# Kernel tuning notes

Hardware: AMD Instinct MI355X
Metric: run time of the kernel (lower is better)

Reference implementation:

```python
import jax, jax.numpy as jnp
import numpy as np
from jax import lax

VOCAB = 50257
S = 96          # seqlen
E = 768         # embedding_dim
H = 768         # lstm hidden
NL = 2          # lstm layers
L = S - 1       # model2 conv blocks (kernel=2, length 96 -> 1)


def setup_inputs() -> dict:
    key = jax.random.key(0)
    ks = jax.random.split(key, 10)
    he = float(np.sqrt(2.0 / (E * 2)))  # He init for kernel-2 relu convs
    return {
        "x": jax.random.randint(ks[0], (1, S), 0, VOCAB),
        "h_state": jnp.zeros((NL, 1, H), jnp.float32),
        "c_state": jnp.zeros((NL, 1, H), jnp.float32),
        "model2_previousOut": jnp.zeros((1, E, 1), jnp.float32),
        "emb1": jax.random.normal(ks[1], (VOCAB, E), jnp.float32),
        "emb2": jax.random.normal(ks[2], (VOCAB, E), jnp.float32),
        "lstm_w_ih": jax.random.normal(ks[3], (NL, 4 * H, E), jnp.float32) * 0.02,
        "lstm_w_hh": jax.random.normal(ks[4], (NL, 4 * H, H), jnp.float32) * 0.02,
        "lstm_b_ih": jnp.zeros((NL, 4 * H), jnp.float32),
        "lstm_b_hh": jnp.zeros((NL, 4 * H), jnp.float32),
        "pred_w": jax.random.normal(ks[5], (1, H * NL), jnp.float32) * 0.02,
        "pred_b": jnp.zeros((1,), jnp.float32),
        "conv_w": jax.random.normal(ks[6], (L, E, E, 2), jnp.float32) * he,
        "conv_b": jnp.zeros((L, E), jnp.float32),
        "m2pred_w": jax.random.normal(ks[7], (1, E, 2), jnp.float32) * 0.02,
        "m2pred_b": jnp.zeros((1,), jnp.float32),
    }


def _lstm_layer(seq, h0, c0, w_ih, w_hh, b_ih, b_hh):
    # seq: [S, in_dim]; torch gate order i, f, g, o
    def step(carry, xt):
        h, c = carry
        g = w_ih @ xt + w_hh @ h + b_ih + b_hh  # [4H]
        i, f, gg, o = jnp.split(g, 4)
        i = jax.nn.sigmoid(i)
        f = jax.nn.sigmoid(f)
        gg = jnp.tanh(gg)
        o = jax.nn.sigmoid(o)
        c = f * c + i * gg
        h = o * jnp.tanh(c)
        return (h, c), h
    (h, c), ys = lax.scan(step, (h0, c0), seq)
    return ys, h, c


def _forward(x, h_state, c_state, model2_previousOut, emb1, emb2,
             lstm_w_ih, lstm_w_hh, lstm_b_ih, lstm_b_hh,
             pred_w, pred_b, conv_w, conv_b, m2pred_w, m2pred_b):
    xb = x[0]                      # [S] token ids (batch=1)
    # ---- model 1: embedding -> 2-layer LSTM -> linear head on final cell states
    seq = emb1[xb]                 # [S, E]
    hs, cs = [], []
    for l in range(NL):
        seq, h, c = _lstm_layer(seq, h_state[l, 0], c_state[l, 0],
                                lstm_w_ih[l], lstm_w_hh[l], lstm_b_ih[l], lstm_b_hh[l])
        hs.append(h)
        cs.append(c)
    h = jnp.stack(hs)[:, None, :]  # [NL, 1, H]
    c = jnp.stack(cs)[:, None, :]  # [NL, 1, H]
    feat = jnp.transpose(c, (1, 2, 0)).reshape(1, H * NL)  # torch permute(1,2,0)+flatten
    out = feat @ pred_w.T + pred_b                          # [1, 1]
    # ---- model 2: embedding -> chain of 95 distinct Conv1d(E,E,2)+ReLU (length 96 -> 1)
    # Fixed-width buffer trick: each layer's position t uses x[t], x[t+1]; only
    # position 0 of the final layer is valid, and it never touches roll wrap-around.
    e2 = emb2[xb].T                # [E, S]
    def cstep(xbuf, wb):
        w, b = wb                  # w: [E, E, 2], b: [E]
        y = jax.nn.relu(w[:, :, 0] @ xbuf + w[:, :, 1] @ jnp.roll(xbuf, -1, axis=1)
                        + b[:, None])
        return y, None
    xbuf, _ = lax.scan(cstep, e2, (conv_w, conv_b))
    model2out = xbuf[None, :, :1]  # [1, E, 1]
    cat = jnp.concatenate([model2out, model2_previousOut], axis=-1)  # [1, E, 2]
    out2 = (jnp.einsum('oek,bek->bo', m2pred_w, cat) + m2pred_b).reshape(1, 1)
    new_prev = model2out.reshape(1, E, 1)
    return out, h, c, out2, new_prev


def reference(x, h_state, c_state, model2_previousOut, emb1, emb2,
              lstm_w_ih, lstm_w_hh, lstm_b_ih, lstm_b_hh,
              pred_w, pred_b, conv_w, conv_b, m2pred_w, m2pred_b):
    return _forward(x, h_state, c_state, model2_previousOut, emb1, emb2,
                    lstm_w_ih, lstm_w_hh, lstm_b_ih, lstm_b_hh,
                    pred_w, pred_b, conv_w, conv_b, m2pred_w, m2pred_b)
```

## Files before the change

kernel.cpp:

```cpp
#include <hip/hip_runtime.h>
#include <math.h>

#define SEQ 96
#define EMB 768
#define G4  3072
#define NLAYER 95
#define CKP 264
#define CONV_WG 48
#define LSTM_WG 192
#define NREP 32
#define XPITCH 1536
#define WB_BYTES 225345536ull

typedef float  f32x4  __attribute__((ext_vector_type(4)));
typedef short  bf16x8 __attribute__((ext_vector_type(8)));
typedef unsigned long long ull;

union BF8 { unsigned short u[8]; bf16x8 v; };

__device__ __forceinline__ unsigned short f2bf(float f) {
    unsigned u = __float_as_uint(f);
    u += 0x7FFFu + ((u >> 16) & 1u);
    return (unsigned short)(u >> 16);
}
__device__ __forceinline__ float bf2f(unsigned short u) {
    return __uint_as_float(((unsigned)u) << 16);
}

__device__ __forceinline__ ull ld64g(const void* p) {
    return __hip_atomic_load((const ull*)p, __ATOMIC_RELAXED,
                             __HIP_MEMORY_SCOPE_AGENT);
}
__device__ __forceinline__ void st32g(void* p, unsigned v) {
    __hip_atomic_store((unsigned*)p, v, __ATOMIC_RELAXED,
                       __HIP_MEMORY_SCOPE_AGENT);
}
__device__ __forceinline__ void stf32g(float* p, float v) {
    __hip_atomic_store((unsigned*)p, __float_as_uint(v), __ATOMIC_RELAXED,
                       __HIP_MEMORY_SCOPE_AGENT);
}
__device__ __forceinline__ unsigned ldflag(const unsigned* p) {
    return __hip_atomic_load(p, __ATOMIC_RELAXED, __HIP_MEMORY_SCOPE_AGENT);
}
__device__ __forceinline__ unsigned ldflag_acq(const unsigned* p) {
    return __hip_atomic_load(p, __ATOMIC_ACQUIRE, __HIP_MEMORY_SCOPE_AGENT);
}
__device__ __forceinline__ void stflag(unsigned* p, unsigned v) {
    __hip_atomic_store(p, v, __ATOMIC_RELAXED, __HIP_MEMORY_SCOPE_AGENT);
}

__device__ __forceinline__ void relbar(unsigned* flags, unsigned* epoch,
                                       int nwg, int wg, unsigned target) {
    asm volatile("s_waitcnt vmcnt(0)" ::: "memory");
    __syncthreads();
    if (threadIdx.x == 0) stflag(&flags[wg * 16], target);
    if (wg == 0) {
        if ((int)threadIdx.x < nwg)
            while (ldflag(&flags[threadIdx.x * 16]) < target)
                __builtin_amdgcn_s_sleep(2);
        __syncthreads();
        if (threadIdx.x < NREP) stflag(&epoch[threadIdx.x * 16], target);
    }
    if (threadIdx.x == 0) {
        const unsigned* ep = &epoch[(wg & (NREP - 1)) * 16];
        while (ldflag(ep) < target)
            __builtin_amdgcn_s_sleep(8);
    }
    asm volatile("" ::: "memory");
    __syncthreads();
}

__device__ __forceinline__ float red16(float a) {
    a += __shfl_xor(a, 8, 16);
    a += __shfl_xor(a, 4, 16);
    a += __shfl_xor(a, 2, 16);
    a += __shfl_xor(a, 1, 16);
    return a;
}

__device__ __forceinline__ float sigmoidf_(float x) {
    return 1.0f / (1.0f + __expf(-x));
}

__global__ void k_prep(const float* __restrict__ w,
                       unsigned short* __restrict__ wb0,
                       unsigned short* __restrict__ wb1) {
    const size_t p0 = ((size_t)blockIdx.x * 256 + threadIdx.x) * 4;
    const f32x4* src = (const f32x4*)(w + p0 * 2);
    f32x4 f0 = __builtin_nontemporal_load(src);
    f32x4 f1 = __builtin_nontemporal_load(src + 1);
    ushort4 a, b;
    a.x = f2bf(f0.x); b.x = f2bf(f0.y);
    a.y = f2bf(f0.z); b.y = f2bf(f0.w);
    a.z = f2bf(f1.x); b.z = f2bf(f1.y);
    a.w = f2bf(f1.z); b.w = f2bf(f1.w);
    *(ushort4*)(wb0 + p0) = a;
    *(ushort4*)(wb1 + p0) = b;
}

__global__ void k_embed(const int* __restrict__ xids,
                        const float* __restrict__ emb2,
                        unsigned short* __restrict__ x0) {
    const int col = blockIdx.x;
    const int tok = xids[col];
    const int tid = threadIdx.x;
    if (tid < 192) {
        float4 v = *(const float4*)(emb2 + (size_t)tok * EMB + tid * 4);
        ushort4 hv, lv;
        hv.x = f2bf(v.x); lv.x = f2bf(v.x - bf2f(hv.x));
        hv.y = f2bf(v.y); lv.y = f2bf(v.y - bf2f(hv.y));
        hv.z = f2bf(v.z); lv.z = f2bf(v.z - bf2f(hv.z));
        hv.w = f2bf(v.w); lv.w = f2bf(v.w - bf2f(hv.w));
        unsigned short* base = x0 + col * XPITCH + (tid >> 2) * 32 + (tid & 3) * 4;
        *(ushort4*)base        = hv;
        *(ushort4*)(base + 16) = lv;
    }
}

#define ISSUE_W_B16(LAY, W0R, W1R) do {                                      \
    const unsigned short* w0_ = wb0 + ((size_t)(LAY) * EMB + r0 + lj) * EMB; \
    const unsigned short* w1_ = wb1 + ((size_t)(LAY) * EMB + r0 + lj) * EMB; \
    _Pragma("unroll")                                                        \
    for (int ch_ = 0; ch_ < 3; ++ch_) {                                      \
        const int k_ = ch_ * 256 + wv * 32 + lg * 8;                         \
        W0R[ch_] = *(const bf16x8*)(w0_ + k_);                               \
        W1R[ch_] = *(const bf16x8*)(w1_ + k_);                               \
    }                                                                        \
} while (0)

#define CONV_BARRIER(LAY, PREFETCH) do {                                     \
    if ((LAY) + 1 < NLAYER) {                                                \
        const unsigned tgt = (unsigned)((LAY) + 1);                          \
        asm volatile("s_waitcnt vmcnt(0)" ::: "memory");                     \
        __syncthreads();                                                     \
        if (tid == 0) stflag(&cflags[bI * 16], tgt);                         \
        PREFETCH;                                                            \
        asm volatile("" ::: "memory");                                       \
        if (bI == 0) {                                                       \
            if (tid < CONV_WG)                                               \
                while (ldflag(&cflags[tid * 16]) < tgt)                      \
                    __builtin_amdgcn_s_sleep(2);                             \
            __syncthreads();                                                 \
            if (tid < NREP) stflag(&cepoch[tid * 16], tgt);                  \
        }                                                                    \
        if (tid == 0) {                                                      \
            const unsigned* ep = &cepoch[(bI & (NREP - 1)) * 16];            \
            while (ldflag(ep) < tgt)                                         \
                __builtin_amdgcn_s_sleep(8);                                 \
            (void)ldflag_acq(ep);              \
        }                                                                    \
        asm volatile("" ::: "memory");                                       \
        __syncthreads();                                                     \
    }                                                                        \
} while (0)

#define CONV_EPILOGUE(LAY) do {                                              \
    _Pragma("unroll")                                                        \
    for (int nt = 0; nt < 6; ++nt) if (nt < nts)                             \
        *(f32x4*)&part[wv * 1536 + (nt * 16 + lj) * 16 + lg * 4] = acc[nt];  \
    __syncthreads();                                                         \
    _Pragma("unroll")                                                        \
    for (int j = 0; j < 2; ++j) {                                            \
        const int o2 = tid + j * 512;                                        \
        const int c = o2 >> 3, p = o2 & 7;                                   \
        if (c < ncols) {                                                     \
            const int i0 = p * 2;                                            \
            const int oo = c * 16 + i0;                                      \
            float s0 = conv_b[(LAY) * EMB + r0 + i0];                        \
            float s1 = conv_b[(LAY) * EMB + r0 + i0 + 1];                    \
            _Pragma("unroll")                                                \
            for (int w = 0; w < 8; ++w) {                                    \
                s0 += part[w * 1536 + oo];                                   \
                s1 += part[w * 1536 + oo + 1];                               \
            }                                                                \
            s0 = fmaxf(s0, 0.f); s1 = fmaxf(s1, 0.f);                        \
            const unsigned short h0 = f2bf(s0), h1 = f2bf(s1);               \
            const unsigned short l0 = f2bf(s0 - bf2f(h0));                   \
            const unsigned short l1 = f2bf(s1 - bf2f(h1));                   \
            unsigned short* dp = dst + c * XPITCH + bI * 32 + i0;            \
            st32g(dp,      (unsigned)h0 | ((unsigned)h1 << 16));             \
            st32g(dp + 16, (unsigned)l0 | ((unsigned)l1 << 16));             \
            if ((LAY) == NLAYER - 1 && c == 0) {                             \
                dout[3074 + r0 + i0]     = s0;                               \
                dout[3074 + r0 + i0 + 1] = s1;                               \
            }                                                                \
        }                                                                    \
    }                                                                        \
} while (0)

#define STAGE_X(CH) do {                                                     \
    _Pragma("unroll")                                                        \
    for (int j = 0; j < 6; ++j) {                                            \
        const int u = tid + j * 512;                                         \
        const int c = u >> 5, q = u & 31;                                    \
        if (c < scols) {                                                     \
            const int k = (CH) * 256 + q * 8;                                \
            const unsigned short* sp =                                       \
                src + c * XPITCH + ((k >> 4) << 5) + (k & 15);               \
            bf16x8 vh = *(const bf16x8*)sp;                     \
            bf16x8 vl = *(const bf16x8*)(sp + 16);              \
            *(bf16x8*)(xs_hi + c * CKP + q * 8) = vh;                        \
            *(bf16x8*)(xs_lo + c * CKP + q * 8) = vl;                        \
        }                                                                    \
    }                                                                        \
} while (0)

#define CONV_CHUNK_B16(CH, W0c, W1c) do {                                    \
    const bf16x8 a0 = W0c[CH];                                               \
    const bf16x8 a1 = W1c[CH];                                               \
    const int klocal = wv * 32;                                              \
    _Pragma("unroll")                                                        \
    for (int nt = 0; nt < 6; ++nt) if (nt < nts) {                           \
        const int co = (nt * 16 + lj) * CKP + klocal + lg * 8;               \
        bf16x8 bh0 = *(const bf16x8*)(xs_hi + co);                           \
        bf16x8 bl0 = *(const bf16x8*)(xs_lo + co);                           \
        bf16x8 bh1 = *(const bf16x8*)(xs_hi + co + CKP);                     \
        bf16x8 bl1 = *(const bf16x8*)(xs_lo + co + CKP);                     \
        acc[nt] = __builtin_amdgcn_mfma_f32_16x16x32_bf16(                   \
                      a0, bh0, acc[nt], 0, 0, 0);                            \
        acc[nt] = __builtin_amdgcn_mfma_f32_16x16x32_bf16(                   \
                      a0, bl0, acc[nt], 0, 0, 0);                            \
        acc[nt] = __builtin_amdgcn_mfma_f32_16x16x32_bf16(                   \
                      a1, bh1, acc[nt], 0, 0, 0);                            \
        acc[nt] = __builtin_amdgcn_mfma_f32_16x16x32_bf16(                   \
                      a1, bl1, acc[nt], 0, 0, 0);                            \
    }                                                                        \
} while (0)

#define CONV_LAYER_B16(LAY, W0c, W1c, W0n, W1n) do {                         \
    const int ncols = NLAYER - (LAY);                                        \
    const int scols = (ncols + 1 < 96) ? ncols + 1 : 96;                     \
    const int nts   = (ncols + 15) >> 4;                                     \
    const unsigned short* src = ((LAY) & 1) ? x1buf : x0buf;                 \
    unsigned short*       dst = ((LAY) & 1) ? x0buf : x1buf;                 \
    f32x4 acc[6];                                                            \
    _Pragma("unroll")                                                        \
    for (int n = 0; n < 6; ++n) acc[n] = (f32x4)0.f;                         \
    _Pragma("unroll")                                                        \
    for (int ch = 0; ch < 3; ++ch) {                                         \
        STAGE_X(ch);                                                         \
        __syncthreads();                                                     \
        CONV_CHUNK_B16(ch, W0c, W1c);                                        \
        __syncthreads();                                                     \
    }                                                                        \
    CONV_EPILOGUE(LAY);                                                      \
    CONV_BARRIER(LAY, ISSUE_W_B16((LAY) + 1, W0n, W1n));                     \
} while (0)

#define ISSUE_W_F32(LAY, WREG) do {                                          \
    const float* wsl_ = conv_w + (size_t)(LAY) * (EMB * EMB * 2)             \
                               + (size_t)(r0 + lj) * (EMB * 2);              \
    _Pragma("unroll")                                                        \
    for (int ch_ = 0; ch_ < 3; ++ch_) {                                      \
        const int K0_ = ch_ * 256 + wv * 32;                                 \
        const float4* ap_ =                                                  \
            (const float4*)(wsl_ + (size_t)(K0_ + lg * 8) * 2);              \
        _Pragma("unroll")                                                    \
        for (int j_ = 0; j_ < 4; ++j_) WREG[ch_][j_] = ap_[j_];              \
    }                                                                        \
} while (0)

#define CONV_LAYER_F32(LAY, Wc, Wn) do {                                     \
    const int ncols = NLAYER - (LAY);                                        \
    const int scols = (ncols + 1 < 96) ? ncols + 1 : 96;                     \
    const int nts   = (ncols + 15) >> 4;                                     \
    const unsigned short* src = ((LAY) & 1) ? x1buf : x0buf;                 \
    unsigned short*       dst = ((LAY) & 1) ? x0buf : x1buf;                 \
    f32x4 acc[6];                                                            \
    _Pragma("unroll")                                                        \
    for (int n = 0; n < 6; ++n) acc[n] = (f32x4)0.f;                         \
    _Pragma("unroll")                                                        \
    for (int ch = 0; ch < 3; ++ch) {                                         \
        STAGE_X(ch);                                                         \
        __syncthreads();                                                     \
        {                                                                    \
            BF8 a0h, a0l, a1h, a1l;                                          \
            _Pragma("unroll")                                                \
            for (int d = 0; d < 8; ++d) {                                    \
                const float4 f = Wc[ch][d >> 1];                             \
                const float w0 = (d & 1) ? f.z : f.x;                        \
                const float w1 = (d & 1) ? f.w : f.y;                        \
                const unsigned short h0 = f2bf(w0);                          \
                const unsigned short h1 = f2bf(w1);                          \
                a0h.u[d] = h0; a0l.u[d] = f2bf(w0 - bf2f(h0));               \
                a1h.u[d] = h1; a1l.u[d] = f2bf(w1 - bf2f(h1));               \
            }                                                                \
            const int klocal = wv * 32;                                      \
            _Pragma("unroll")                                                \
            for (int nt = 0; nt < 6; ++nt) if (nt < nts) {                   \
                const int co = (nt * 16 + lj) * CKP + klocal + lg * 8;       \
                bf16x8 bh0 = *(const bf16x8*)(xs_hi + co);                   \
                bf16x8 bl0 = *(const bf16x8*)(xs_lo + co);                   \
                bf16x8 bh1 = *(const bf16x8*)(xs_hi + co + CKP);             \
                bf16x8 bl1 = *(const bf16x8*)(xs_lo + co + CKP);             \
                acc[nt] = __builtin_amdgcn_mfma_f32_16x16x32_bf16(           \
                              a0h.v, bh0, acc[nt], 0, 0, 0);                 \
                acc[nt] = __builtin_amdgcn_mfma_f32_16x16x32_bf16(           \
                              a0h.v, bl0, acc[nt], 0, 0, 0);                 \
                acc[nt] = __builtin_amdgcn_mfma_f32_16x16x32_bf16(           \
                              a0l.v, bh0, acc[nt], 0, 0, 0);                 \
                acc[nt] = __builtin_amdgcn_mfma_f32_16x16x32_bf16(           \
                              a1h.v, bh1, acc[nt], 0, 0, 0);                 \
                acc[nt] = __builtin_amdgcn_mfma_f32_16x16x32_bf16(           \
                              a1h.v, bl1, acc[nt], 0, 0, 0);                 \
                acc[nt] = __builtin_amdgcn_mfma_f32_16x16x32_bf16(           \
                              a1l.v, bh1, acc[nt], 0, 0, 0);                 \
            }                                                                \
        }                                                                    \
        __syncthreads();                                                     \
    }                                                                        \
    CONV_EPILOGUE(LAY);                                                      \
    CONV_BARRIER(LAY, ISSUE_W_F32((LAY) + 1, Wn));                           \
} while (0)

__global__ __launch_bounds__(512, 1) void k_net(
    const int use_b16,
    const int* __restrict__ xids, const float* __restrict__ emb1,
    const float* __restrict__ conv_w, const float* __restrict__ conv_b,
    const unsigned short* __restrict__ wb0,
    const unsigned short* __restrict__ wb1,
    unsigned short* __restrict__ x0buf, unsigned short* __restrict__ x1buf,
    const float* __restrict__ hstate, const float* __restrict__ cstate,
    const float* __restrict__ wih, const float* __restrict__ whh,
    const float* __restrict__ bih, const float* __restrict__ bhh,
    float* __restrict__ h1buf, float* __restrict__ h2buf,
    unsigned* __restrict__ cflags, unsigned* __restrict__ cepoch,
    unsigned* __restrict__ lflags, unsigned* __restrict__ lepoch,
    float* __restrict__ dout) {

    __shared__ __align__(16) unsigned short xs_hi[97 * CKP];
    __shared__ __align__(16) unsigned short xs_lo[97 * CKP];
    __shared__ __align__(16) float hx[EMB], hb2[EMB], ex[EMB];
    __shared__ float g1s[16], g2s[16], c1s[4], c2s[4];
    float* part = (float*)xs_hi;

    const int tid = threadIdx.x;

    if (blockIdx.x < CONV_WG) {
        const int wv = tid >> 6;
        const int ln = tid & 63;
        const int lj = ln & 15;
        const int lg = ln >> 4;
        const int bI = blockIdx.x;
        const int r0 = bI * 16;

        if (use_b16) {
            bf16x8 W0a[3], W1a[3], W0b[3], W1b[3];
            ISSUE_W_B16(0, W0a, W1a);
#pragma unroll 1
            for (int lay = 0; lay + 1 < NLAYER; lay += 2) {
                CONV_LAYER_B16(lay, W0a, W1a, W0b, W1b);
                CONV_LAYER_B16(lay + 1, W0b, W1b, W0a, W1a);
            }
            CONV_LAYER_B16(NLAYER - 1, W0a, W1a, W0b, W1b);
        } else {
            float4 Wa[3][4], Wb[3][4];
            ISSUE_W_F32(0, Wa);
#pragma unroll 1
            for (int lay = 0; lay + 1 < NLAYER; lay += 2) {
                CONV_LAYER_F32(lay, Wa, Wb);
                CONV_LAYER_F32(lay + 1, Wb, Wa);
            }
            CONV_LAYER_F32(NLAYER - 1, Wa, Wb);
        }
    } else {
        const int wg   = blockIdx.x - CONV_WG;
        const bool act = tid < 256;
        const int l16  = tid & 15;
        const int r16  = (tid & 255) >> 4;
        const int gate = r16 >> 2;
        const int jl   = r16 & 3;
        const int j0   = wg * 4;
        const int grow = gate * EMB + j0 + jl;

        float wi1r[48], wh1r[48], wi2r[48], wh2r[48];
        float b1 = 0.f, b2 = 0.f;
        if (act) {
            const float* wih1 = wih;
            const float* whh1 = whh;
            const float* wih2 = wih + (size_t)G4 * EMB;
            const float* whh2 = whh + (size_t)G4 * EMB;
#pragma unroll
            for (int i = 0; i < 48; ++i) {
                const int k = l16 + (i << 4);
                wi1r[i] = wih1[(size_t)grow * EMB + k];
                wh1r[i] = whh1[(size_t)grow * EMB + k];
                wi2r[i] = wih2[(size_t)grow * EMB + k];
                wh2r[i] = whh2[(size_t)grow * EMB + k];
            }
            b1 = bih[grow] + bhh[grow];
            b2 = bih[G4 + grow] + bhh[G4 + grow];
        }

        if (tid < 4)      c1s[tid]     = cstate[j0 + tid];
        else if (tid < 8) c2s[tid - 4] = cstate[EMB + j0 + (tid - 4)];
        __syncthreads();

        for (int T = 0; T <= SEQ; ++T) {
            if (tid < 192) {
                if (T < SEQ) {
                    const int tok = xids[T];
                    float4 v = *(const float4*)(emb1 + (size_t)tok * EMB + tid * 4);
                    *(float4*)(ex + tid * 4) = v;
                }
                ull a0, a1;
                if (T == 0) {
                    a0 = ld64g(hstate + tid * 4);
                    a1 = ld64g(hstate + tid * 4 + 2);
                } else {
                    a0 = ld64g(h1buf + (T - 1) * EMB + tid * 4);
                    a1 = ld64g(h1buf + (T - 1) * EMB + tid * 4 + 2);
                }
                *(ull*)(hx + tid * 4)     = a0;
                *(ull*)(hx + tid * 4 + 2) = a1;
                ull b0 = 0, b1v = 0;
                if (T >= 1) {
                    if (T == 1) {
                        b0  = ld64g(hstate + EMB + tid * 4);
                        b1v = ld64g(hstate + EMB + tid * 4 + 2);
                    } else {
                        b0  = ld64g(h2buf + (T - 2) * EMB + tid * 4);
                        b1v = ld64g(h2buf + (T - 2) * EMB + tid * 4 + 2);
                    }
                }
                *(ull*)(hb2 + tid * 4)     = b0;
                *(ull*)(hb2 + tid * 4 + 2) = b1v;
            }
            __syncthreads();

            if (act && T < SEQ) {
                float a = b1;
#pragma unroll
                for (int i = 0; i < 48; ++i)
                    a = fmaf(wi1r[i], ex[l16 + (i << 4)], a);
#pragma unroll
                for (int i = 0; i < 48; ++i)
                    a = fmaf(wh1r[i], hx[l16 + (i << 4)], a);
                a = red16(a);
                if (l16 == 0) g1s[r16] = a;
            }
            if (act && T >= 1) {
                float b = b2;
#pragma unroll
                for (int i = 0; i < 48; ++i)
                    b = fmaf(wi2r[i], hx[l16 + (i << 4)], b);
#pragma unroll
                for (int i = 0; i < 48; ++i)
                    b = fmaf(wh2r[i], hb2[l16 + (i << 4)], b);
                b = red16(b);
                if (l16 == 0) g2s[r16] = b;
            }
            __syncthreads();

            if (tid < 4 && T < SEQ) {
                const int j = tid;
                const float i_ = sigmoidf_(g1s[j]);
                const float f_ = sigmoidf_(g1s[4 + j]);
                const float g_ = tanhf(g1s[8 + j]);
                const float o_ = sigmoidf_(g1s[12 + j]);
                const float c  = f_ * c1s[j] + i_ * g_;
                c1s[j] = c;
                const float h = o_ * tanhf(c);
                stf32g(&h1buf[T * EMB + j0 + j], h);
                if (T == SEQ - 1) {
                    dout[1 + j0 + j]    = h;
                    dout[1537 + j0 + j] = c;
                }
            } else if (tid >= 4 && tid < 8 && T >= 1) {
                const int j = tid - 4;
                const int s = T - 1;
                const float i_ = sigmoidf_(g2s[j]);
                const float f_ = sigmoidf_(g2s[4 + j]);
                const float g_ = tanhf(g2s[8 + j]);
                const float o_ = sigmoidf_(g2s[12 + j]);
                const float c  = f_ * c2s[j] + i_ * g_;
                c2s[j] = c;
                const float h = o_ * tanhf(c);
                stf32g(&h2buf[s * EMB + j0 + j], h);
                if (s == SEQ - 1) {
                    dout[1 + EMB + j0 + j]    = h;
                    dout[1537 + EMB + j0 + j] = c;
                }
            }
            if (T < SEQ)
                relbar(lflags, lepoch, LSTM_WG, wg, (unsigned)(T + 1));
        }
    }
}

__global__ void k_final(const float* __restrict__ pred_w,
                        const float* __restrict__ pred_b,
                        const float* __restrict__ m2w,
                        const float* __restrict__ m2b,
                        const float* __restrict__ prev,
                        float* __restrict__ dout) {
    __shared__ float red[256];
    const int tid = threadIdx.x;
    float p1 = 0.f;
    for (int idx = tid; idx < 2 * EMB; idx += 256) {
        const int l = idx / EMB;
        const int j = idx - l * EMB;
        p1 += dout[1537 + idx] * pred_w[j * 2 + l];
    }
    float p2 = 0.f;
    for (int e = tid; e < EMB; e += 256)
        p2 += dout[3074 + e] * m2w[2 * e] + prev[e] * m2w[2 * e + 1];

    red[tid] = p1;
    __syncthreads();
    for (int s = 128; s > 0; s >>= 1) {
        if (tid < s) red[tid] += red[tid + s];
        __syncthreads();
    }
    if (tid == 0) dout[0] = red[0] + pred_b[0];
    __syncthreads();
    red[tid] = p2;
    __syncthreads();
    for (int s = 128; s > 0; s >>= 1) {
        if (tid < s) red[tid] += red[tid + s];
        __syncthreads();
    }
    if (tid == 0) dout[3073] = red[0] + m2b[0];
}

extern "C" void kernel_launch(void* const* d_in, const int* in_sizes, int n_in,
                              void* d_out, int out_size, void* d_ws, size_t ws_size,
                              hipStream_t stream) {
    const int*   x      = (const int*)d_in[0];
    const float* hstate = (const float*)d_in[1];
    const float* cstate = (const float*)d_in[2];
    const float* prev   = (const float*)d_in[3];
    const float* emb1   = (const float*)d_in[4];
    const float* emb2   = (const float*)d_in[5];
    const float* wih    = (const float*)d_in[6];
    const float* whh    = (const float*)d_in[7];
    const float* bih    = (const float*)d_in[8];
    const float* bhh    = (const float*)d_in[9];
    const float* predw  = (const float*)d_in[10];
    const float* predb  = (const float*)d_in[11];
    const float* convw  = (const float*)d_in[12];
    const float* convb  = (const float*)d_in[13];
    const float* m2w    = (const float*)d_in[14];
    const float* m2b    = (const float*)d_in[15];
    float* out = (float*)d_out;

    char* wsb = (char*)d_ws;
    unsigned* wsw = (unsigned*)d_ws;
    unsigned* cflags = wsw;
    unsigned* cepoch = wsw + 1024;
    unsigned* lflags = wsw + 2048;
    unsigned* lepoch = wsw + 6144;
    float* h1buf = (float*)(wsb + 32768);
    float* h2buf = (float*)(wsb + 32768 + 294912);
    unsigned short* x0buf = (unsigned short*)(wsb + 622592);
    unsigned short* x1buf = (unsigned short*)(wsb + 917504);
    unsigned short* wb0   = (unsigned short*)(wsb + 1212416);
    unsigned short* wb1   = (unsigned short*)(wsb + 113278976);
    const int use_b16 = (ws_size >= WB_BYTES) ? 1 : 0;

    hipMemsetAsync(d_ws, 0, 32768, stream);
    hipMemsetAsync(d_out, 0, out_size * sizeof(float), stream);

    if (use_b16)
        k_prep<<<54720, 256, 0, stream>>>(convw, wb0, wb1);
    k_embed<<<96, 256, 0, stream>>>(x, emb2, x0buf);
    k_net<<<CONV_WG + LSTM_WG, 512, 0, stream>>>(
        use_b16, x, emb1, convw, convb, wb0, wb1, x0buf, x1buf,
        hstate, cstate, wih, whh, bih, bhh, h1buf, h2buf,
        cflags, cepoch, lflags, lepoch, out);
    k_final<<<1, 256, 0, stream>>>(predw, predb, m2w, m2b, prev, out);
}
```

Before: 950.7 us.

## Spread conv layers over 64 workgroups with 12 output rows each

Increases the number of conv workgroups from 48 to 64, each now owning 12 output channels instead of 16. MFMA lanes with lj>=12 load no weights and keep zeroed registers, so the per-workgroup weight streaming is reduced and spread over more CUs. The epilogue index math is reworked for 6 pairs per column and for non-16-aligned row groups. The cost is wasted MFMA lanes, more participants in the per-layer cross-workgroup barrier, and possibly fewer CUs left for the LSTM workgroups.

```diff
diff --git a/kernel.cpp b/kernel.cpp
--- a/kernel.cpp
+++ b/kernel.cpp
@@ -6,7 +6,7 @@
 #define G4  3072
 #define NLAYER 95
 #define CKP 264
-#define CONV_WG 48
+#define CONV_WG 64
 #define LSTM_WG 192
 #define NREP 32
 #define XPITCH 1536
@@ -118,13 +118,17 @@
 }
 
 #define ISSUE_W_B16(LAY, W0R, W1R) do {                                      \
-    const unsigned short* w0_ = wb0 + ((size_t)(LAY) * EMB + r0 + lj) * EMB; \
-    const unsigned short* w1_ = wb1 + ((size_t)(LAY) * EMB + r0 + lj) * EMB; \
-    _Pragma("unroll")                                                        \
-    for (int ch_ = 0; ch_ < 3; ++ch_) {                                      \
-        const int k_ = ch_ * 256 + wv * 32 + lg * 8;                         \
-        W0R[ch_] = *(const bf16x8*)(w0_ + k_);                               \
-        W1R[ch_] = *(const bf16x8*)(w1_ + k_);                               \
+    if (lj < 12) {                                                           \
+        const unsigned short* w0_ =                                          \
+            wb0 + ((size_t)(LAY) * EMB + r0 + lj) * EMB;                     \
+        const unsigned short* w1_ =                                          \
+            wb1 + ((size_t)(LAY) * EMB + r0 + lj) * EMB;                     \
+        _Pragma("unroll")                                                    \
+        for (int ch_ = 0; ch_ < 3; ++ch_) {                                  \
+            const int k_ = ch_ * 256 + wv * 32 + lg * 8;                     \
+            W0R[ch_] = *(const bf16x8*)(w0_ + k_);                           \
+            W1R[ch_] = *(const bf16x8*)(w1_ + k_);                           \
+        }                                                                    \
     }                                                                        \
 } while (0)
 
@@ -162,8 +166,9 @@
     _Pragma("unroll")                                                        \
     for (int j = 0; j < 2; ++j) {                                            \
         const int o2 = tid + j * 512;                                        \
-        const int c = o2 >> 3, p = o2 & 7;                                   \
-        if (c < ncols) {                                                     \
+        if (o2 < ncols * 6) {                                                \
+            const int c = (o2 * 683) >> 12;                                  \
+            const int p = o2 - c * 6;                                        \
             const int i0 = p * 2;                                            \
             const int oo = c * 16 + i0;                                      \
             float s0 = conv_b[(LAY) * EMB + r0 + i0];                        \
@@ -177,12 +182,14 @@
             const unsigned short h0 = f2bf(s0), h1 = f2bf(s1);               \
             const unsigned short l0 = f2bf(s0 - bf2f(h0));                   \
             const unsigned short l1 = f2bf(s1 - bf2f(h1));                   \
-            unsigned short* dp = dst + c * XPITCH + bI * 32 + i0;            \
+            const int rg = r0 + i0;                                          \
+            unsigned short* dp = dst + c * XPITCH + ((rg >> 4) << 5)         \
+                                     + (rg & 15);                            \
             st32g(dp,      (unsigned)h0 | ((unsigned)h1 << 16));             \
             st32g(dp + 16, (unsigned)l0 | ((unsigned)l1 << 16));             \
             if ((LAY) == NLAYER - 1 && c == 0) {                             \
-                dout[3074 + r0 + i0]     = s0;                               \
-                dout[3074 + r0 + i0 + 1] = s1;                               \
+                dout[3074 + rg]     = s0;                                    \
+                dout[3074 + rg + 1] = s1;                                    \
             }                                                                \
         }                                                                    \
     }                                                                        \
@@ -248,15 +255,17 @@
 } while (0)
 
 #define ISSUE_W_F32(LAY, WREG) do {                                          \
-    const float* wsl_ = conv_w + (size_t)(LAY) * (EMB * EMB * 2)             \
-                               + (size_t)(r0 + lj) * (EMB * 2);              \
-    _Pragma("unroll")                                                        \
-    for (int ch_ = 0; ch_ < 3; ++ch_) {                                      \
-        const int K0_ = ch_ * 256 + wv * 32;                                 \
-        const float4* ap_ =                                                  \
-            (const float4*)(wsl_ + (size_t)(K0_ + lg * 8) * 2);              \
+    if (lj < 12) {                                                           \
+        const float* wsl_ = conv_w + (size_t)(LAY) * (EMB * EMB * 2)         \
+                                   + (size_t)(r0 + lj) * (EMB * 2);          \
         _Pragma("unroll")                                                    \
-        for (int j_ = 0; j_ < 4; ++j_) WREG[ch_][j_] = ap_[j_];              \
+        for (int ch_ = 0; ch_ < 3; ++ch_) {                                  \
+            const int K0_ = ch_ * 256 + wv * 32;                             \
+            const float4* ap_ =                                              \
+                (const float4*)(wsl_ + (size_t)(K0_ + lg * 8) * 2);          \
+            _Pragma("unroll")                                                \
+            for (int j_ = 0; j_ < 4; ++j_) WREG[ch_][j_] = ap_[j_];          \
+        }                                                                    \
     }                                                                        \
 } while (0)
 
@@ -342,10 +351,18 @@
         const int lj = ln & 15;
         const int lg = ln >> 4;
         const int bI = blockIdx.x;
-        const int r0 = bI * 16;
+        const int r0 = bI * 12;
 
         if (use_b16) {
+            BF8 zz;
+#pragma unroll
+            for (int d = 0; d < 8; ++d) zz.u[d] = 0;
             bf16x8 W0a[3], W1a[3], W0b[3], W1b[3];
+#pragma unroll
+            for (int c = 0; c < 3; ++c) {
+                W0a[c] = zz.v; W1a[c] = zz.v;
+                W0b[c] = zz.v; W1b[c] = zz.v;
+            }
             ISSUE_W_B16(0, W0a, W1a);
 #pragma unroll 1
             for (int lay = 0; lay + 1 < NLAYER; lay += 2) {
@@ -355,6 +372,13 @@
             CONV_LAYER_B16(NLAYER - 1, W0a, W1a, W0b, W1b);
         } else {
             float4 Wa[3][4], Wb[3][4];
+#pragma unroll
+            for (int c = 0; c < 3; ++c)
+#pragma unroll
+                for (int j = 0; j < 4; ++j) {
+                    Wa[c][j] = make_float4(0.f, 0.f, 0.f, 0.f);
+                    Wb[c][j] = make_float4(0.f, 0.f, 0.f, 0.f);
+                }
             ISSUE_W_F32(0, Wa);
 #pragma unroll 1
             for (int lay = 0; lay + 1 < NLAYER; lay += 2) {
```

After: 944.1 us. No clear change (-0.7%).
